# Kernel tuning notes

Measured on AMD Instinct MI355X. Metric: run time of the kernel, lower is better.

The kernel has to match this reference:

```python
import jax, jax.numpy as jnp
import numpy as np

NX, NY, NT = 128, 128, 64          # global space-time grid
LX, LY = 2.0, 2.0                  # periodic domain extents
K_NB = 128                         # neighbors per query
NHEAD = 4
EPS = 1e-5


def setup_inputs() -> dict:
    key = jax.random.key(0)
    ks = jax.random.split(key, 12)
    N = NX * NY * NT
    B, d, dff, L = 2048, 64, 128, 2
    nrm = lambda k, s: jax.random.normal(k, s, jnp.float32) * 0.05
    return {
        "q_lin_idx": jax.random.randint(ks[0], (B,), 0, N),
        "offsets_ijk": jax.random.randint(ks[1], (K_NB, 3), 0, 8),
        "coords": jax.random.uniform(ks[2], (N, 3), jnp.float32) * 2.0,
        "vals": jax.random.normal(ks[3], (N, 3), jnp.float32),
        "log_gammas": jnp.zeros((3,), jnp.float32),
        "proj_w": nrm(ks[4], (d, 6)), "proj_b": jnp.zeros((d,), jnp.float32),
        "qkv_w": nrm(ks[5], (L, 3 * d, d)), "qkv_b": jnp.zeros((L, 3 * d), jnp.float32),
        "out_w": nrm(ks[6], (L, d, d)), "out_b": jnp.zeros((L, d), jnp.float32),
        "ln1_s": jnp.ones((L, d), jnp.float32), "ln1_b": jnp.zeros((L, d), jnp.float32),
        "ff1_w": nrm(ks[7], (L, dff, d)), "ff1_b": jnp.zeros((L, dff), jnp.float32),
        "ff2_w": nrm(ks[8], (L, d, dff)), "ff2_b": jnp.zeros((L, d), jnp.float32),
        "ln2_s": jnp.ones((L, d), jnp.float32), "ln2_b": jnp.zeros((L, d), jnp.float32),
        "head_ln_s": jnp.ones((d,), jnp.float32), "head_ln_b": jnp.zeros((d,), jnp.float32),
        "head1_w": nrm(ks[9], (d, d)), "head1_b": jnp.zeros((d,), jnp.float32),
        "head2_w": nrm(ks[10], (3, d)), "head2_b": jnp.zeros((3,), jnp.float32),
    }


def _ln(x, s, b):
    m = x.mean(-1, keepdims=True)
    v = ((x - m) ** 2).mean(-1, keepdims=True)
    return (x - m) * jax.lax.rsqrt(v + EPS) * s + b


def _dper(a, b, L):
    # periodic relative delta in [-L/2, L/2)
    return (a - b + 0.5 * L) % L - 0.5 * L


def reference(q_lin_idx, offsets_ijk, coords, vals, log_gammas, proj_w, proj_b,
              qkv_w, qkv_b, out_w, out_b, ln1_s, ln1_b, ff1_w, ff1_b, ff2_w, ff2_b,
              ln2_s, ln2_b, head_ln_s, head_ln_b, head1_w, head1_b, head2_w, head2_b):
    # --- periodic-wrapped neighbor indices (div/mod on linear index) ---
    i = q_lin_idx // (NY * NT)
    r = q_lin_idx % (NY * NT)
    j = r // NT
    kk = r % NT
    di, dj, dk = offsets_ijk[:, 0], offsets_ijk[:, 1], offsets_ijk[:, 2]
    I = (i[:, None] + di[None, :]) % NX          # wrap_x
    J = (j[:, None] + dj[None, :]) % NY          # wrap_y
    T = jnp.clip(kk[:, None] + dk[None, :], 0, NT - 1)  # no wrap in t
    nb = I * (NY * NT) + J * NT + T              # [B, K]

    # --- gather + relative-delta encode ---
    q_xyz = coords[q_lin_idx]                    # [B, 3]
    nb_xyz = coords[nb]                          # [B, K, 3]
    dx = _dper(nb_xyz[..., 0], q_xyz[:, None, 0], LX)
    dy = _dper(nb_xyz[..., 1], q_xyz[:, None, 1], LY)
    dt = nb_xyz[..., 2] - q_xyz[:, None, 2]
    rel = jnp.stack([dx, dy, dt], -1) * jnp.exp(log_gammas)[None, None, :]
    tokens = jnp.concatenate([rel, vals[nb]], -1)  # [B, K, 6]

    # --- input projection + TransformerEncoder (post-norm, relu FF) ---
    h = tokens @ proj_w.T + proj_b               # [B, S, d]
    B, S, d = h.shape
    dh = d // NHEAD
    scale = 1.0 / np.sqrt(dh).astype(np.float32)
    for l in range(qkv_w.shape[0]):
        qkv = h @ qkv_w[l].T + qkv_b[l]
        qh, kh, vh = jnp.split(qkv, 3, axis=-1)
        qh = qh.reshape(B, S, NHEAD, dh).transpose(0, 2, 1, 3)
        kh = kh.reshape(B, S, NHEAD, dh).transpose(0, 2, 1, 3)
        vh = vh.reshape(B, S, NHEAD, dh).transpose(0, 2, 1, 3)
        att = jax.nn.softmax(jnp.einsum('bhqd,bhkd->bhqk', qh, kh) * scale, axis=-1)
        o = jnp.einsum('bhqk,bhkd->bhqd', att, vh).transpose(0, 2, 1, 3).reshape(B, S, d)
        h = _ln(h + (o @ out_w[l].T + out_b[l]), ln1_s[l], ln1_b[l])
        ff = jax.nn.relu(h @ ff1_w[l].T + ff1_b[l]) @ ff2_w[l].T + ff2_b[l]
        h = _ln(h + ff, ln2_s[l], ln2_b[l])

    # --- mean pool over neighbors + head ---
    hm = h.mean(axis=1)                          # [B, d]
    g = _ln(hm, head_ln_s, head_ln_b)
    g = jax.nn.gelu(g @ head1_w.T + head1_b, approximate=False)
    return g @ head2_w.T + head2_b               # [B, 3]
```

## Files before the change

kernel.cpp:

```cpp
#include <hip/hip_runtime.h>
#include <math.h>

#define NXg 128
#define NYg 128
#define NTg 64
#define SEQ 128
#define DIM 64
#define NH 4
#define DHd 16
#define DFFd 128
#define NLAYER 2
#define EPSf 1e-5f

typedef _Float16 f16x8 __attribute__((ext_vector_type(8)));
typedef _Float16 f16x4 __attribute__((ext_vector_type(4)));
typedef __fp16 fp16x2 __attribute__((ext_vector_type(2)));
typedef float f32x4 __attribute__((ext_vector_type(4)));

#define MFMA16(a, b, c) __builtin_amdgcn_mfma_f32_16x16x32_f16(a, b, c, 0, 0, 0)

union FragU { int d[4]; f16x8 v; };
union H4U  { int d[2]; f16x4 v; };
union P2U  { int i; fp16x2 h; };

__device__ __forceinline__ int pk2(float a, float b) {
  P2U u;
  u.h = __builtin_amdgcn_cvt_pkrtz(a, b);
  return u.i;
}
__device__ __forceinline__ float2 up2(int p) {
  P2U u; u.i = p;
  return make_float2((float)u.h[0], (float)u.h[1]);
}

__device__ __forceinline__ f16x8 zero8() {
  f16x8 z;
#pragma unroll
  for (int i = 0; i < 8; ++i) z[i] = (_Float16)0.0f;
  return z;
}
__device__ __forceinline__ f32x4 zero4f() {
  f32x4 z;
  z[0] = 0.f; z[1] = 0.f; z[2] = 0.f; z[3] = 0.f;
  return z;
}
__device__ __forceinline__ f16x8 ld8(const _Float16* p) { return *(const f16x8*)p; }

__device__ __forceinline__ f16x8 frag_k16(f32x4 d4, int quad, int l15) {
  int p0 = pk2(d4[0], d4[1]);
  int p1 = pk2(d4[2], d4[3]);
  int slA = ((2 * quad) * 16 + l15) & 63;
  int slB = ((2 * quad + 1) * 16 + l15) & 63;
  FragU u;
  u.d[0] = __shfl(p0, slA, 64);
  u.d[1] = __shfl(p1, slA, 64);
  u.d[2] = __shfl(p0, slB, 64);
  u.d[3] = __shfl(p1, slB, 64);
  if (quad >= 2) { u.d[0] = 0; u.d[1] = 0; u.d[2] = 0; u.d[3] = 0; }
  return u.v;
}

__device__ __forceinline__ f16x8 frag_k64(const int pk[8], int kt, int quad, int l15) {
  const int slA = (2 * (quad & 1)) * 16 + l15;
  const int slB = (2 * (quad & 1) + 1) * 16 + l15;
  const bool hi = quad >= 2;
  int a0 = __shfl(pk[4 * kt + 0], slA, 64), b0 = __shfl(pk[4 * kt + 2], slA, 64);
  int a1 = __shfl(pk[4 * kt + 1], slA, 64), b1 = __shfl(pk[4 * kt + 3], slA, 64);
  int a2 = __shfl(pk[4 * kt + 0], slB, 64), b2 = __shfl(pk[4 * kt + 2], slB, 64);
  int a3 = __shfl(pk[4 * kt + 1], slB, 64), b3 = __shfl(pk[4 * kt + 3], slB, 64);
  FragU u;
  u.d[0] = hi ? b0 : a0;
  u.d[1] = hi ? b1 : a1;
  u.d[2] = hi ? b2 : a2;
  u.d[3] = hi ? b3 : a3;
  return u.v;
}

__device__ __forceinline__ void res_ln_qt(const f32x4 acc[4], int pkX[8],
                                          const float* __restrict__ bias,
                                          const float* __restrict__ lns,
                                          const float* __restrict__ lnb,
                                          int quad) {
  float v[4][4];
  float s = 0.f;
#pragma unroll
  for (int mt = 0; mt < 4; ++mt) {
    f32x4 bb = *(const f32x4*)(bias + mt * 16 + quad * 4);
    float2 x0 = up2(pkX[mt * 2 + 0]);
    float2 x1 = up2(pkX[mt * 2 + 1]);
    v[mt][0] = acc[mt][0] + bb[0] + x0.x;
    v[mt][1] = acc[mt][1] + bb[1] + x0.y;
    v[mt][2] = acc[mt][2] + bb[2] + x1.x;
    v[mt][3] = acc[mt][3] + bb[3] + x1.y;
    s += (v[mt][0] + v[mt][1]) + (v[mt][2] + v[mt][3]);
  }
  s += __shfl_xor(s, 16, 64);
  s += __shfl_xor(s, 32, 64);
  const float mu = s * (1.0f / 64.0f);
  float q2 = 0.f;
#pragma unroll
  for (int mt = 0; mt < 4; ++mt)
#pragma unroll
    for (int jr = 0; jr < 4; ++jr) { float d = v[mt][jr] - mu; q2 = fmaf(d, d, q2); }
  q2 += __shfl_xor(q2, 16, 64);
  q2 += __shfl_xor(q2, 32, 64);
  const float rstd = rsqrtf(q2 * (1.0f / 64.0f) + EPSf);
#pragma unroll
  for (int mt = 0; mt < 4; ++mt) {
    f32x4 sv = *(const f32x4*)(lns + mt * 16 + quad * 4);
    f32x4 bv = *(const f32x4*)(lnb + mt * 16 + quad * 4);
    float o0 = fmaf((v[mt][0] - mu) * rstd, sv[0], bv[0]);
    float o1 = fmaf((v[mt][1] - mu) * rstd, sv[1], bv[1]);
    float o2 = fmaf((v[mt][2] - mu) * rstd, sv[2], bv[2]);
    float o3 = fmaf((v[mt][3] - mu) * rstd, sv[3], bv[3]);
    pkX[mt * 2 + 0] = pk2(o0, o1);
    pkX[mt * 2 + 1] = pk2(o2, o3);
  }
}

__global__ void prep_weights(const float* __restrict__ qkv_w,
                             const float* __restrict__ out_w,
                             const float* __restrict__ ff1_w,
                             const float* __restrict__ ff2_w,
                             _Float16* __restrict__ wsH) {
  int i = blockIdx.x * 256 + threadIdx.x;
  if (i < 24576) wsH[i] = (_Float16)qkv_w[i];
  else if (i < 32768) wsH[i] = (_Float16)out_w[i - 24576];
  else if (i < 49152) wsH[i] = (_Float16)ff1_w[i - 32768];
  else if (i < 65536) wsH[i] = (_Float16)ff2_w[i - 49152];
}

__global__ __launch_bounds__(256, 3)
void fieldformer_mfma(const int* __restrict__ q_lin_idx,
                      const int* __restrict__ offsets_ijk,
                      const float* __restrict__ coords,
                      const float* __restrict__ vals,
                      const float* __restrict__ log_gammas,
                      const float* __restrict__ proj_w,
                      const float* __restrict__ proj_b,
                      const float* __restrict__ qkv_b,
                      const float* __restrict__ out_b,
                      const float* __restrict__ ln1_s,
                      const float* __restrict__ ln1_b,
                      const float* __restrict__ ff1_b,
                      const float* __restrict__ ff2_b,
                      const float* __restrict__ ln2_s,
                      const float* __restrict__ ln2_b,
                      const float* __restrict__ head_ln_s,
                      const float* __restrict__ head_ln_b,
                      const float* __restrict__ head1_w,
                      const float* __restrict__ head1_b,
                      const float* __restrict__ head2_w,
                      const float* __restrict__ head2_b,
                      const _Float16* __restrict__ wH,
                      float* __restrict__ out) {
  __shared__ __align__(16) _Float16 sPH[128 * 136];
  __shared__ __align__(16) _Float16 sK[128 * 24];
  __shared__ __align__(16) _Float16 sV[16 * 136];

  const int tid = threadIdx.x;
  const int wv = tid >> 6;
  const int lane = tid & 63;
  const int quad = lane >> 4;
  const int l15 = lane & 15;
  const int b = blockIdx.x;

  {
    const int row = tid >> 1, hf = tid & 1;
    const int q = q_lin_idx[b];
    const int qi = q / (NYg * NTg);
    const int qrem = q - qi * (NYg * NTg);
    const int qj = qrem / NTg;
    const int qk = qrem - qj * NTg;
    const int di = offsets_ijk[row * 3 + 0];
    const int dj = offsets_ijk[row * 3 + 1];
    const int dk = offsets_ijk[row * 3 + 2];
    const int I = (qi + di) % NXg;
    const int J = (qj + dj) % NYg;
    int T = qk + dk; T = T < 0 ? 0 : (T > NTg - 1 ? NTg - 1 : T);
    const int nb = I * (NYg * NTg) + J * NTg + T;
    const float qx = coords[q * 3 + 0], qy = coords[q * 3 + 1], qz = coords[q * 3 + 2];
    const float nx_ = coords[nb * 3 + 0], ny_ = coords[nb * 3 + 1], nz_ = coords[nb * 3 + 2];
    float ax = nx_ - qx + 1.0f; ax -= 2.0f * floorf(ax * 0.5f); ax -= 1.0f;
    float ay = ny_ - qy + 1.0f; ay -= 2.0f * floorf(ay * 0.5f); ay -= 1.0f;
    const float at = nz_ - qz;
    float tok[6];
    tok[0] = ax * expf(log_gammas[0]);
    tok[1] = ay * expf(log_gammas[1]);
    tok[2] = at * expf(log_gammas[2]);
    tok[3] = vals[nb * 3 + 0];
    tok[4] = vals[nb * 3 + 1];
    tok[5] = vals[nb * 3 + 2];
#pragma unroll
    for (int ci = 0; ci < 32; ++ci) {
      const int c = hf * 32 + ci;
      const float* w = proj_w + c * 6;
      float a = proj_b[c];
      a = fmaf(tok[0], w[0], a); a = fmaf(tok[1], w[1], a);
      a = fmaf(tok[2], w[2], a); a = fmaf(tok[3], w[3], a);
      a = fmaf(tok[4], w[4], a); a = fmaf(tok[5], w[5], a);
      sPH[row * 136 + c] = (_Float16)a;
    }
  }
  __syncthreads();

  int pkX[2][8];
#pragma unroll
  for (int qt = 0; qt < 2; ++qt) {
    const int q = (wv * 2 + qt) * 16 + l15;
#pragma unroll
    for (int mt = 0; mt < 4; ++mt) {
      int2 t = *(const int2*)(sPH + q * 136 + mt * 16 + quad * 4);
      pkX[qt][mt * 2 + 0] = t.x;
      pkX[qt][mt * 2 + 1] = t.y;
    }
  }

  for (int l = 0; l < NLAYER; ++l) {
    const _Float16* qkvH = wH + l * 192 * 64;
    const _Float16* woutH = wH + 24576 + l * 64 * 64;
    const _Float16* ff1H = wH + 32768 + l * 128 * 64;
    const _Float16* ff2H = wH + 49152 + l * 64 * 128;
    const float* bqkv = qkv_b + l * 192;

    f16x8 bxf[2][2];
#pragma unroll
    for (int qt = 0; qt < 2; ++qt)
#pragma unroll
      for (int kt = 0; kt < 2; ++kt) bxf[qt][kt] = frag_k64(pkX[qt], kt, quad, l15);

    f32x4 y2[2][4];
#pragma unroll
    for (int qt = 0; qt < 2; ++qt)
#pragma unroll
      for (int mt = 0; mt < 4; ++mt) y2[qt][mt] = zero4f();

    for (int h = 0; h < NH; ++h) {
      f32x4 dq[2] = {zero4f(), zero4f()};
      f32x4 dk[2] = {zero4f(), zero4f()};
      f32x4 dv[2] = {zero4f(), zero4f()};
#pragma unroll
      for (int kt = 0; kt < 2; ++kt) {
        f16x8 awq = ld8(qkvH + (h * 16 + l15) * 64 + kt * 32 + quad * 8);
        f16x8 awk = ld8(qkvH + (64 + h * 16 + l15) * 64 + kt * 32 + quad * 8);
        f16x8 awv = ld8(qkvH + (128 + h * 16 + l15) * 64 + kt * 32 + quad * 8);
#pragma unroll
        for (int qt = 0; qt < 2; ++qt) {
          dq[qt] = MFMA16(awq, bxf[qt][kt], dq[qt]);
          dk[qt] = MFMA16(awk, bxf[qt][kt], dk[qt]);
          dv[qt] = MFMA16(awv, bxf[qt][kt], dv[qt]);
        }
      }
      f16x8 bqf[2];
      {
        const f32x4 bq4 = *(const f32x4*)(bqkv + h * 16 + quad * 4);
        const f32x4 bk4 = *(const f32x4*)(bqkv + 64 + h * 16 + quad * 4);
        const f32x4 bv4 = *(const f32x4*)(bqkv + 128 + h * 16 + quad * 4);
#pragma unroll
        for (int qt = 0; qt < 2; ++qt) {
          const int q = (wv * 2 + qt) * 16 + l15;
          H4U k4;
          k4.d[0] = pk2(dk[qt][0] + bk4[0], dk[qt][1] + bk4[1]);
          k4.d[1] = pk2(dk[qt][2] + bk4[2], dk[qt][3] + bk4[3]);
          *(f16x4*)(sK + q * 24 + quad * 4) = k4.v;
#pragma unroll
          for (int jr = 0; jr < 4; ++jr)
            sV[(quad * 4 + jr) * 136 + q] = (_Float16)(dv[qt][jr] + bv4[jr]);
          f32x4 qv;
#pragma unroll
          for (int jr = 0; jr < 4; ++jr) qv[jr] = (dq[qt][jr] + bq4[jr]) * 0.25f;
          bqf[qt] = frag_k16(qv, quad, l15);
        }
      }
      __syncthreads();

#pragma unroll
      for (int qt = 0; qt < 2; ++qt) {
        const int q = (wv * 2 + qt) * 16 + l15;
        float s0 = 0.f;
#pragma unroll
        for (int mt = 0; mt < 8; ++mt) {
          f16x8 ak = (quad < 2) ? ld8(sK + (mt * 16 + l15) * 24 + quad * 8) : zero8();
          f32x4 zc = zero4f();
          f32x4 sc = MFMA16(ak, bqf[qt], zc);
          float e0 = __expf(sc[0]), e1 = __expf(sc[1]);
          float e2 = __expf(sc[2]), e3 = __expf(sc[3]);
          s0 += (e0 + e1) + (e2 + e3);
          H4U pp;
          pp.d[0] = pk2(e0, e1);
          pp.d[1] = pk2(e2, e3);
          *(f16x4*)(sPH + q * 136 + mt * 16 + quad * 4) = pp.v;
        }
        s0 += __shfl_xor(s0, 16, 64);
        s0 += __shfl_xor(s0, 32, 64);
        const float inv = 1.0f / s0;
        f32x4 ov = zero4f();
#pragma unroll
        for (int kt = 0; kt < 4; ++kt) {
          f16x8 av = ld8(sV + l15 * 136 + kt * 32 + quad * 8);
          f16x8 bp = ld8(sPH + q * 136 + kt * 32 + quad * 8);
          ov = MFMA16(av, bp, ov);
        }
#pragma unroll
        for (int jr = 0; jr < 4; ++jr) ov[jr] *= inv;
        f16x8 bof = frag_k16(ov, quad, l15);
#pragma unroll
        for (int mt = 0; mt < 4; ++mt) {
          f16x8 aw = (quad < 2) ? ld8(woutH + (mt * 16 + l15) * 64 + h * 16 + quad * 8)
                                : zero8();
          y2[qt][mt] = MFMA16(aw, bof, y2[qt][mt]);
        }
      }
      __syncthreads();
    }

#pragma unroll
    for (int qt = 0; qt < 2; ++qt)
      res_ln_qt(y2[qt], pkX[qt], out_b + l * 64, ln1_s + l * 64, ln1_b + l * 64, quad);

#pragma unroll
    for (int qt = 0; qt < 2; ++qt)
#pragma unroll
      for (int kt = 0; kt < 2; ++kt) bxf[qt][kt] = frag_k64(pkX[qt], kt, quad, l15);

#pragma unroll
    for (int qt = 0; qt < 2; ++qt) {
      const int q = (wv * 2 + qt) * 16 + l15;
      const float* b1 = ff1_b + l * 128;
#pragma unroll
      for (int mt = 0; mt < 8; ++mt) {
        f32x4 f8 = zero4f();
#pragma unroll
        for (int kt = 0; kt < 2; ++kt) {
          f16x8 aw = ld8(ff1H + (mt * 16 + l15) * 64 + kt * 32 + quad * 8);
          f8 = MFMA16(aw, bxf[qt][kt], f8);
        }
        f32x4 bb = *(const f32x4*)(b1 + mt * 16 + quad * 4);
        H4U hh;
        hh.d[0] = pk2(fmaxf(f8[0] + bb[0], 0.f), fmaxf(f8[1] + bb[1], 0.f));
        hh.d[1] = pk2(fmaxf(f8[2] + bb[2], 0.f), fmaxf(f8[3] + bb[3], 0.f));
        *(f16x4*)(sPH + q * 136 + mt * 16 + quad * 4) = hh.v;
      }
    }

#pragma unroll
    for (int qt = 0; qt < 2; ++qt) {
      const int q = (wv * 2 + qt) * 16 + l15;
      f32x4 g4[4];
#pragma unroll
      for (int mt = 0; mt < 4; ++mt) g4[mt] = zero4f();
#pragma unroll
      for (int kt = 0; kt < 4; ++kt) {
        f16x8 bh = ld8(sPH + q * 136 + kt * 32 + quad * 8);
#pragma unroll
        for (int mt = 0; mt < 4; ++mt) {
          f16x8 aw = ld8(ff2H + (mt * 16 + l15) * 128 + kt * 32 + quad * 8);
          g4[mt] = MFMA16(aw, bh, g4[mt]);
        }
      }
      res_ln_qt(g4, pkX[qt], ff2_b + l * 64, ln2_s + l * 64, ln2_b + l * 64, quad);
    }
  }

  __syncthreads();
  {
    float* pf = (float*)sK;
    float* gsc = pf + 256;
    float* asc = gsc + 64;
    f32x4 cs[4];
#pragma unroll
    for (int mt = 0; mt < 4; ++mt) {
      float2 a0 = up2(pkX[0][mt * 2 + 0]), a1 = up2(pkX[0][mt * 2 + 1]);
      float2 b0 = up2(pkX[1][mt * 2 + 0]), b1 = up2(pkX[1][mt * 2 + 1]);
      cs[mt][0] = a0.x + b0.x;
      cs[mt][1] = a0.y + b0.y;
      cs[mt][2] = a1.x + b1.x;
      cs[mt][3] = a1.y + b1.y;
    }
#pragma unroll
    for (int d = 1; d <= 8; d <<= 1)
#pragma unroll
      for (int mt = 0; mt < 4; ++mt)
#pragma unroll
        for (int jr = 0; jr < 4; ++jr) cs[mt][jr] += __shfl_xor(cs[mt][jr], d, 64);
    if (l15 == 0) {
#pragma unroll
      for (int mt = 0; mt < 4; ++mt)
        *(f32x4*)(pf + wv * 64 + mt * 16 + quad * 4) = cs[mt];
    }
    __syncthreads();
    if (tid < 64) {
      const float hm = (pf[tid] + pf[64 + tid] + pf[128 + tid] + pf[192 + tid]) * (1.0f / 128.0f);
      float t = hm;
      t += __shfl_xor(t, 1, 64);  t += __shfl_xor(t, 2, 64);
      t += __shfl_xor(t, 4, 64);  t += __shfl_xor(t, 8, 64);
      t += __shfl_xor(t, 16, 64); t += __shfl_xor(t, 32, 64);
      const float mu = t * (1.0f / 64.0f);
      const float dv = hm - mu;
      float v2 = dv * dv;
      v2 += __shfl_xor(v2, 1, 64);  v2 += __shfl_xor(v2, 2, 64);
      v2 += __shfl_xor(v2, 4, 64);  v2 += __shfl_xor(v2, 8, 64);
      v2 += __shfl_xor(v2, 16, 64); v2 += __shfl_xor(v2, 32, 64);
      const float var = v2 * (1.0f / 64.0f);
      gsc[tid] = fmaf(dv * rsqrtf(var + EPSf), head_ln_s[tid], head_ln_b[tid]);
    }
    __syncthreads();
    if (tid < 64) {
      float z = head1_b[tid];
      for (int k = 0; k < 64; ++k) z = fmaf(gsc[k], head1_w[tid * 64 + k], z);
      asc[tid] = 0.5f * z * (1.0f + erff(z * 0.70710678118654752f));
    }
    __syncthreads();
    if (tid < 3) {
      float z = head2_b[tid];
      for (int k = 0; k < 64; ++k) z = fmaf(asc[k], head2_w[tid * 64 + k], z);
      out[b * 3 + tid] = z;
    }
  }
}

extern "C" void kernel_launch(void* const* d_in, const int* in_sizes, int n_in,
                              void* d_out, int out_size, void* d_ws, size_t ws_size,
                              hipStream_t stream) {
  (void)n_in; (void)ws_size; (void)out_size;
  const int B = in_sizes[0];
  _Float16* wsH = (_Float16*)d_ws;

  prep_weights<<<dim3(256), dim3(256), 0, stream>>>(
      (const float*)d_in[7],
      (const float*)d_in[9],
      (const float*)d_in[13],
      (const float*)d_in[15],
      wsH);

  fieldformer_mfma<<<dim3(B), dim3(256), 0, stream>>>(
      (const int*)d_in[0],
      (const int*)d_in[1],
      (const float*)d_in[2],
      (const float*)d_in[3],
      (const float*)d_in[4],
      (const float*)d_in[5],
      (const float*)d_in[6],
      (const float*)d_in[8],
      (const float*)d_in[10],
      (const float*)d_in[11],
      (const float*)d_in[12],
      (const float*)d_in[14],
      (const float*)d_in[16],
      (const float*)d_in[17],
      (const float*)d_in[18],
      (const float*)d_in[19],
      (const float*)d_in[20],
      (const float*)d_in[21],
      (const float*)d_in[22],
      (const float*)d_in[23],
      (const float*)d_in[24],
      wsH,
      (float*)d_out);
}
```

Before: 380.8 us.

## Compute all heads' QKV at once and keep P/FF activations in registers

The attention loop now computes Q, K and V for all four heads in one pass and stores K and V for every head in widened shared buffers. This replaces the two block barriers per head with one barrier per layer. The softmax probabilities and FF1 activations stay in registers and are turned into MFMA operands with cross-lane shuffles instead of a round trip through shared memory. The output projection becomes a single full-K GEMM after all heads finish. The cost is more registers and shuffles, and the occupancy hint drops from 3 to 2 blocks per CU.

```diff
diff --git a/kernel.cpp b/kernel.cpp
--- a/kernel.cpp
+++ b/kernel.cpp
@@ -46,9 +46,7 @@
 }
 __device__ __forceinline__ f16x8 ld8(const _Float16* p) { return *(const f16x8*)p; }
 
-__device__ __forceinline__ f16x8 frag_k16(f32x4 d4, int quad, int l15) {
-  int p0 = pk2(d4[0], d4[1]);
-  int p1 = pk2(d4[2], d4[3]);
+__device__ __forceinline__ f16x8 frag_k16p(int p0, int p1, int quad, int l15) {
   int slA = ((2 * quad) * 16 + l15) & 63;
   int slB = ((2 * quad + 1) * 16 + l15) & 63;
   FragU u;
@@ -60,7 +58,7 @@
   return u.v;
 }
 
-__device__ __forceinline__ f16x8 frag_k64(const int pk[8], int kt, int quad, int l15) {
+__device__ __forceinline__ f16x8 frag_k64(const int* pk, int kt, int quad, int l15) {
   const int slA = (2 * (quad & 1)) * 16 + l15;
   const int slB = (2 * (quad & 1) + 1) * 16 + l15;
   const bool hi = quad >= 2;
@@ -130,7 +128,7 @@
   else if (i < 65536) wsH[i] = (_Float16)ff2_w[i - 49152];
 }
 
-__global__ __launch_bounds__(256, 3)
+__global__ __launch_bounds__(256, 2)
 void fieldformer_mfma(const int* __restrict__ q_lin_idx,
                       const int* __restrict__ offsets_ijk,
                       const float* __restrict__ coords,
@@ -154,9 +152,8 @@
                       const float* __restrict__ head2_b,
                       const _Float16* __restrict__ wH,
                       float* __restrict__ out) {
-  __shared__ __align__(16) _Float16 sPH[128 * 136];
-  __shared__ __align__(16) _Float16 sK[128 * 24];
-  __shared__ __align__(16) _Float16 sV[16 * 136];
+  __shared__ __align__(16) _Float16 sK[128 * 72];
+  __shared__ __align__(16) _Float16 sV[64 * 136];
 
   const int tid = threadIdx.x;
   const int wv = tid >> 6;
@@ -199,7 +196,7 @@
       a = fmaf(tok[0], w[0], a); a = fmaf(tok[1], w[1], a);
       a = fmaf(tok[2], w[2], a); a = fmaf(tok[3], w[3], a);
       a = fmaf(tok[4], w[4], a); a = fmaf(tok[5], w[5], a);
-      sPH[row * 136 + c] = (_Float16)a;
+      sK[row * 72 + c] = (_Float16)a;
     }
   }
   __syncthreads();
@@ -210,7 +207,7 @@
     const int q = (wv * 2 + qt) * 16 + l15;
 #pragma unroll
     for (int mt = 0; mt < 4; ++mt) {
-      int2 t = *(const int2*)(sPH + q * 136 + mt * 16 + quad * 4);
+      int2 t = *(const int2*)(sK + q * 72 + mt * 16 + quad * 4);
       pkX[qt][mt * 2 + 0] = t.x;
       pkX[qt][mt * 2 + 1] = t.y;
     }
@@ -223,27 +220,25 @@
     const _Float16* ff2H = wH + 49152 + l * 64 * 128;
     const float* bqkv = qkv_b + l * 192;
 
+    __syncthreads();
+
     f16x8 bxf[2][2];
 #pragma unroll
     for (int qt = 0; qt < 2; ++qt)
 #pragma unroll
       for (int kt = 0; kt < 2; ++kt) bxf[qt][kt] = frag_k64(pkX[qt], kt, quad, l15);
 
-    f32x4 y2[2][4];
-#pragma unroll
-    for (int qt = 0; qt < 2; ++qt)
-#pragma unroll
-      for (int mt = 0; mt < 4; ++mt) y2[qt][mt] = zero4f();
-
-    for (int h = 0; h < NH; ++h) {
+    int pkQ[2][8];
+#pragma unroll
+    for (int hd = 0; hd < NH; ++hd) {
       f32x4 dq[2] = {zero4f(), zero4f()};
       f32x4 dk[2] = {zero4f(), zero4f()};
       f32x4 dv[2] = {zero4f(), zero4f()};
 #pragma unroll
       for (int kt = 0; kt < 2; ++kt) {
-        f16x8 awq = ld8(qkvH + (h * 16 + l15) * 64 + kt * 32 + quad * 8);
-        f16x8 awk = ld8(qkvH + (64 + h * 16 + l15) * 64 + kt * 32 + quad * 8);
-        f16x8 awv = ld8(qkvH + (128 + h * 16 + l15) * 64 + kt * 32 + quad * 8);
+        f16x8 awq = ld8(qkvH + (hd * 16 + l15) * 64 + kt * 32 + quad * 8);
+        f16x8 awk = ld8(qkvH + (64 + hd * 16 + l15) * 64 + kt * 32 + quad * 8);
+        f16x8 awv = ld8(qkvH + (128 + hd * 16 + l15) * 64 + kt * 32 + quad * 8);
 #pragma unroll
         for (int qt = 0; qt < 2; ++qt) {
           dq[qt] = MFMA16(awq, bxf[qt][kt], dq[qt]);
@@ -251,107 +246,98 @@
           dv[qt] = MFMA16(awv, bxf[qt][kt], dv[qt]);
         }
       }
-      f16x8 bqf[2];
-      {
-        const f32x4 bq4 = *(const f32x4*)(bqkv + h * 16 + quad * 4);
-        const f32x4 bk4 = *(const f32x4*)(bqkv + 64 + h * 16 + quad * 4);
-        const f32x4 bv4 = *(const f32x4*)(bqkv + 128 + h * 16 + quad * 4);
-#pragma unroll
-        for (int qt = 0; qt < 2; ++qt) {
-          const int q = (wv * 2 + qt) * 16 + l15;
-          H4U k4;
-          k4.d[0] = pk2(dk[qt][0] + bk4[0], dk[qt][1] + bk4[1]);
-          k4.d[1] = pk2(dk[qt][2] + bk4[2], dk[qt][3] + bk4[3]);
-          *(f16x4*)(sK + q * 24 + quad * 4) = k4.v;
-#pragma unroll
-          for (int jr = 0; jr < 4; ++jr)
-            sV[(quad * 4 + jr) * 136 + q] = (_Float16)(dv[qt][jr] + bv4[jr]);
-          f32x4 qv;
-#pragma unroll
-          for (int jr = 0; jr < 4; ++jr) qv[jr] = (dq[qt][jr] + bq4[jr]) * 0.25f;
-          bqf[qt] = frag_k16(qv, quad, l15);
-        }
-      }
-      __syncthreads();
-
+      const f32x4 bq4 = *(const f32x4*)(bqkv + hd * 16 + quad * 4);
+      const f32x4 bk4 = *(const f32x4*)(bqkv + 64 + hd * 16 + quad * 4);
+      const f32x4 bv4 = *(const f32x4*)(bqkv + 128 + hd * 16 + quad * 4);
 #pragma unroll
       for (int qt = 0; qt < 2; ++qt) {
         const int q = (wv * 2 + qt) * 16 + l15;
+        H4U k4;
+        k4.d[0] = pk2(dk[qt][0] + bk4[0], dk[qt][1] + bk4[1]);
+        k4.d[1] = pk2(dk[qt][2] + bk4[2], dk[qt][3] + bk4[3]);
+        *(f16x4*)(sK + q * 72 + hd * 16 + quad * 4) = k4.v;
+#pragma unroll
+        for (int jr = 0; jr < 4; ++jr)
+          sV[(hd * 16 + quad * 4 + jr) * 136 + q] = (_Float16)(dv[qt][jr] + bv4[jr]);
+        pkQ[qt][hd * 2 + 0] = pk2((dq[qt][0] + bq4[0]) * 0.25f, (dq[qt][1] + bq4[1]) * 0.25f);
+        pkQ[qt][hd * 2 + 1] = pk2((dq[qt][2] + bq4[2]) * 0.25f, (dq[qt][3] + bq4[3]) * 0.25f);
+      }
+    }
+    __syncthreads();
+
+    int pkO[2][8];
+#pragma unroll
+    for (int hd = 0; hd < NH; ++hd) {
+#pragma unroll
+      for (int qt = 0; qt < 2; ++qt) {
+        f16x8 bqf = frag_k16p(pkQ[qt][hd * 2 + 0], pkQ[qt][hd * 2 + 1], quad, l15);
         float s0 = 0.f;
+        int pkP[16];
 #pragma unroll
         for (int mt = 0; mt < 8; ++mt) {
-          f16x8 ak = (quad < 2) ? ld8(sK + (mt * 16 + l15) * 24 + quad * 8) : zero8();
+          f16x8 ak = (quad < 2) ? ld8(sK + (mt * 16 + l15) * 72 + hd * 16 + quad * 8)
+                                : zero8();
           f32x4 zc = zero4f();
-          f32x4 sc = MFMA16(ak, bqf[qt], zc);
+          f32x4 sc = MFMA16(ak, bqf, zc);
           float e0 = __expf(sc[0]), e1 = __expf(sc[1]);
           float e2 = __expf(sc[2]), e3 = __expf(sc[3]);
           s0 += (e0 + e1) + (e2 + e3);
-          H4U pp;
-          pp.d[0] = pk2(e0, e1);
-          pp.d[1] = pk2(e2, e3);
-          *(f16x4*)(sPH + q * 136 + mt * 16 + quad * 4) = pp.v;
+          pkP[mt * 2 + 0] = pk2(e0, e1);
+          pkP[mt * 2 + 1] = pk2(e2, e3);
         }
         s0 += __shfl_xor(s0, 16, 64);
         s0 += __shfl_xor(s0, 32, 64);
         const float inv = 1.0f / s0;
         f32x4 ov = zero4f();
 #pragma unroll
-        for (int kt = 0; kt < 4; ++kt) {
-          f16x8 av = ld8(sV + l15 * 136 + kt * 32 + quad * 8);
-          f16x8 bp = ld8(sPH + q * 136 + kt * 32 + quad * 8);
+        for (int kt2 = 0; kt2 < 4; ++kt2) {
+          f16x8 av = ld8(sV + (hd * 16 + l15) * 136 + kt2 * 32 + quad * 8);
+          f16x8 bp = frag_k64(pkP + 8 * (kt2 >> 1), kt2 & 1, quad, l15);
           ov = MFMA16(av, bp, ov);
         }
-#pragma unroll
-        for (int jr = 0; jr < 4; ++jr) ov[jr] *= inv;
-        f16x8 bof = frag_k16(ov, quad, l15);
+        pkO[qt][hd * 2 + 0] = pk2(ov[0] * inv, ov[1] * inv);
+        pkO[qt][hd * 2 + 1] = pk2(ov[2] * inv, ov[3] * inv);
+      }
+    }
+
+#pragma unroll
+    for (int qt = 0; qt < 2; ++qt) {
+      f32x4 y2[4] = {zero4f(), zero4f(), zero4f(), zero4f()};
+#pragma unroll
+      for (int kt = 0; kt < 2; ++kt) {
+        f16x8 bof = frag_k64(pkO[qt], kt, quad, l15);
 #pragma unroll
         for (int mt = 0; mt < 4; ++mt) {
-          f16x8 aw = (quad < 2) ? ld8(woutH + (mt * 16 + l15) * 64 + h * 16 + quad * 8)
-                                : zero8();
-          y2[qt][mt] = MFMA16(aw, bof, y2[qt][mt]);
-        }
-      }
-      __syncthreads();
-    }
-
-#pragma unroll
-    for (int qt = 0; qt < 2; ++qt)
-      res_ln_qt(y2[qt], pkX[qt], out_b + l * 64, ln1_s + l * 64, ln1_b + l * 64, quad);
-
-#pragma unroll
-    for (int qt = 0; qt < 2; ++qt)
-#pragma unroll
-      for (int kt = 0; kt < 2; ++kt) bxf[qt][kt] = frag_k64(pkX[qt], kt, quad, l15);
+          f16x8 aw = ld8(woutH + (mt * 16 + l15) * 64 + kt * 32 + quad * 8);
+          y2[mt] = MFMA16(aw, bof, y2[mt]);
+        }
+      }
+      res_ln_qt(y2, pkX[qt], out_b + l * 64, ln1_s + l * 64, ln1_b + l * 64, quad);
+    }
 
 #pragma unroll
     for (int qt = 0; qt < 2; ++qt) {
-      const int q = (wv * 2 + qt) * 16 + l15;
+      f16x8 bx2[2];
+#pragma unroll
+      for (int kt = 0; kt < 2; ++kt) bx2[kt] = frag_k64(pkX[qt], kt, quad, l15);
       const float* b1 = ff1_b + l * 128;
+      int pkH[16];
 #pragma unroll
       for (int mt = 0; mt < 8; ++mt) {
         f32x4 f8 = zero4f();
 #pragma unroll
         for (int kt = 0; kt < 2; ++kt) {
           f16x8 aw = ld8(ff1H + (mt * 16 + l15) * 64 + kt * 32 + quad * 8);
-          f8 = MFMA16(aw, bxf[qt][kt], f8);
+          f8 = MFMA16(aw, bx2[kt], f8);
         }
         f32x4 bb = *(const f32x4*)(b1 + mt * 16 + quad * 4);
-        H4U hh;
-        hh.d[0] = pk2(fmaxf(f8[0] + bb[0], 0.f), fmaxf(f8[1] + bb[1], 0.f));
-        hh.d[1] = pk2(fmaxf(f8[2] + bb[2], 0.f), fmaxf(f8[3] + bb[3], 0.f));
-        *(f16x4*)(sPH + q * 136 + mt * 16 + quad * 4) = hh.v;
-      }
-    }
-
-#pragma unroll
-    for (int qt = 0; qt < 2; ++qt) {
-      const int q = (wv * 2 + qt) * 16 + l15;
-      f32x4 g4[4];
-#pragma unroll
-      for (int mt = 0; mt < 4; ++mt) g4[mt] = zero4f();
+        pkH[mt * 2 + 0] = pk2(fmaxf(f8[0] + bb[0], 0.f), fmaxf(f8[1] + bb[1], 0.f));
+        pkH[mt * 2 + 1] = pk2(fmaxf(f8[2] + bb[2], 0.f), fmaxf(f8[3] + bb[3], 0.f));
+      }
+      f32x4 g4[4] = {zero4f(), zero4f(), zero4f(), zero4f()};
 #pragma unroll
       for (int kt = 0; kt < 4; ++kt) {
-        f16x8 bh = ld8(sPH + q * 136 + kt * 32 + quad * 8);
+        f16x8 bh = frag_k64(pkH + 8 * (kt >> 1), kt & 1, quad, l15);
 #pragma unroll
         for (int mt = 0; mt < 4; ++mt) {
           f16x8 aw = ld8(ff2H + (mt * 16 + l15) * 128 + kt * 32 + quad * 8);
```

Result: faster. 342.7 us (-10.0%).
